# Kernel tuning notes

Hardware: AMD Instinct MI355X
Metric: run time of the kernel (lower is better)

The kernel has to match this reference:

```python
import jax, jax.numpy as jnp
import numpy as np

H, KVH, D = 32, 8, 128          # heads, kv heads, head dim
WINDOW = 512                     # sliding_window
NEG = -1e30


def _rotate_half(x):
    x1, x2 = jnp.split(x, 2, axis=-1)
    return jnp.concatenate([-x2, x1], axis=-1)


def setup_inputs() -> dict:
    key = jax.random.key(0)
    ks = jax.random.split(key, 6)
    B, S = 4, 1024
    T = B * S
    hidden = H * D  # 4096
    # RoPE tables [max_pos, head_dim]
    inv_freq = 1.0 / (10000.0 ** (jnp.arange(0, D, 2, dtype=jnp.float32) / D))
    freqs = jnp.outer(jnp.arange(S, dtype=jnp.float32), inv_freq)
    emb = jnp.concatenate([freqs, freqs], axis=-1)
    cos, sin = jnp.cos(emb), jnp.sin(emb)
    x = jax.random.normal(ks[0], (T, hidden), dtype=jnp.float32)
    pos = jnp.tile(jnp.arange(S, dtype=jnp.int64), B)            # positions restart per seq
    cu = jnp.arange(B + 1, dtype=jnp.int32) * S                  # uniform varlen offsets
    sc = 0.02
    Wq = jax.random.normal(ks[1], (hidden, H * D), jnp.float32) * sc
    Wk = jax.random.normal(ks[2], (hidden, KVH * D), jnp.float32) * sc
    Wv = jax.random.normal(ks[3], (hidden, KVH * D), jnp.float32) * sc
    Wo = jax.random.normal(ks[4], (H * D, hidden), jnp.float32) * sc
    return {"cos": cos, "sin": sin, "nz_hidden_states": x,
            "nz_position_ids": pos, "cu_seqlens": cu, "max_seqlen": S,
            "Wq": Wq, "Wk": Wk, "Wv": Wv, "Wo": Wo}


def reference(cos, sin, nz_hidden_states, nz_position_ids, cu_seqlens, max_seqlen,
              Wq, Wk, Wv, Wo):
    T = nz_hidden_states.shape[0]
    q = (nz_hidden_states @ Wq).reshape(T, H, D)
    k = (nz_hidden_states @ Wk).reshape(T, KVH, D)
    v = (nz_hidden_states @ Wv).reshape(T, KVH, D)
    # RoPE: gather by position, broadcast over head dim (unsqueeze(-2))
    c = cos[nz_position_ids][:, None, :]
    s = sin[nz_position_ids][:, None, :]
    q = q * c + _rotate_half(q) * s
    k = k * c + _rotate_half(k) * s
    # uniform varlen -> batch view [B, S, ...]
    B = cu_seqlens.shape[0] - 1
    S = T // B
    G = H // KVH  # query heads per kv head (GQA)
    qb = q.reshape(B, S, KVH, G, D)
    kb = k.reshape(B, S, KVH, D)
    vb = v.reshape(B, S, KVH, D)
    scores = jnp.einsum('bqhgd,bkhd->bhgqk', qb, kb) / jnp.sqrt(jnp.float32(D))
    i = jnp.arange(S)[:, None]
    j = jnp.arange(S)[None, :]
    mask = (j <= i) & (i - j <= WINDOW)  # causal + sliding window
    scores = jnp.where(mask, scores, NEG)
    p = jax.nn.softmax(scores, axis=-1)
    out = jnp.einsum('bhgqk,bkhd->bqhgd', p, vb).reshape(T, H * D)
    return out @ Wo
```

## Files before the change

kernel.cpp:

```cpp
#include <hip/hip_runtime.h>

typedef __bf16 bf16_t;
typedef __bf16 bf16x8 __attribute__((ext_vector_type(8)));
typedef __bf16 bf16x4 __attribute__((ext_vector_type(4)));
typedef float  f32x4  __attribute__((ext_vector_type(4)));
typedef float  f32x16 __attribute__((ext_vector_type(16)));
typedef unsigned int u32x4 __attribute__((ext_vector_type(4)));

#define N_HEADS 32
#define N_KVH   8
#define HEADDIM 128
#define WINDOW  512
#define NBATCH  4
#define SEQLEN  1024
#define NTOK    (NBATCH * SEQLEN)
#define HIDDEN  4096
#define QKVW    6144

__device__ __forceinline__ void llds16(const bf16_t* g, const bf16_t* l)
{
    __builtin_amdgcn_global_load_lds(
        (const __attribute__((address_space(1))) void*)g,
        (__attribute__((address_space(3))) void*)l, 16, 0, 0);
}

template<bool OUT_F32>
__global__ __launch_bounds__(512, 4)
void gemm_dual_kernel(const bf16_t* __restrict__ A, const bf16_t* __restrict__ Bt,
                      void* __restrict__ Cp, int M, int N, int K)
{
    __shared__ __align__(16) char lds[3 * 24576];
    const int tid  = threadIdx.x;
    const int w    = tid >> 6, lane = tid & 63;
    const int ntx  = N >> 7;
    const int nwg  = gridDim.x;
    const int cpx  = nwg >> 3;
    const int lin  = blockIdx.x;
    const int swz  = (nwg & 7) == 0 ? (lin & 7) * cpx + (lin >> 3) : lin;
    const int m0   = (swz / ntx) * 256;
    const int n0   = (swz % ntx) * 128;
    const int wm   = (w >> 1) * 64;
    const int wn   = (w & 1) * 64;
    const int fr   = lane & 15;
    const int kslot16 = (((lane >> 4) ^ ((lane >> 1) & 3)) << 4);
    const int srcblk  = (((tid & 3) ^ ((tid >> 3) & 3)) << 3);
    const int nk = K >> 5;

    f32x4 acc[4][4];
#pragma unroll
    for (int i = 0; i < 4; ++i)
#pragma unroll
        for (int j = 0; j < 4; ++j) {
            acc[i][j][0] = 0.f; acc[i][j][1] = 0.f;
            acc[i][j][2] = 0.f; acc[i][j][3] = 0.f;
        }

    const bf16_t* arow = A  + (size_t)(m0 + (tid >> 2)) * K + srcblk;
    const bf16_t* brow = Bt + (size_t)(n0 + (tid >> 2)) * K + srcblk;
    const size_t rowK128 = (size_t)128 * K;

    auto STAGE = [&](int tt, int buf) {
        char* dst = lds + buf * 24576 + w * 1024;
        const int kt = tt << 5;
        llds16(arow + kt,           (const bf16_t*)(dst));
        llds16(arow + rowK128 + kt, (const bf16_t*)(dst + 8192));
        llds16(brow + kt,           (const bf16_t*)(dst + 16384));
    };

    STAGE(0, 0); STAGE(1, 1);

    int cur = 0;
    for (int t = 0; t < nk; ++t) {
        if (t + 1 < nk) asm volatile("s_waitcnt vmcnt(3)" ::: "memory");
        else            asm volatile("s_waitcnt vmcnt(0)" ::: "memory");
        __builtin_amdgcn_sched_barrier(0);
        __builtin_amdgcn_s_barrier();
        __builtin_amdgcn_sched_barrier(0);

        const char* base = lds + cur * 24576;
        bf16x8 af[4], bfg[4];
#pragma unroll
        for (int mt = 0; mt < 4; ++mt)
            af[mt] = *(const bf16x8*)(base + ((wm + mt * 16 + fr) << 6) + kslot16);
#pragma unroll
        for (int nt = 0; nt < 4; ++nt)
            bfg[nt] = *(const bf16x8*)(base + 16384 + ((wn + nt * 16 + fr) << 6) + kslot16);

        if (t + 2 < nk) {
            int nb = cur + 2; if (nb >= 3) nb -= 3;
            STAGE(t + 2, nb);
        }
        __builtin_amdgcn_s_setprio(1);
#pragma unroll
        for (int mt = 0; mt < 4; ++mt)
#pragma unroll
            for (int nt = 0; nt < 4; ++nt)
                acc[mt][nt] = __builtin_amdgcn_mfma_f32_16x16x32_bf16(
                    af[mt], bfg[nt], acc[mt][nt], 0, 0, 0);
        __builtin_amdgcn_s_setprio(0);
        ++cur; if (cur == 3) cur = 0;
    }

    const int r0 = (lane >> 4) << 2;
#pragma unroll
    for (int mt = 0; mt < 4; ++mt)
#pragma unroll
        for (int nt = 0; nt < 4; ++nt)
#pragma unroll
            for (int r = 0; r < 4; ++r) {
                int row = m0 + wm + mt * 16 + r0 + r;
                int col = n0 + wn + nt * 16 + fr;
                if constexpr (OUT_F32)
                    ((float*)Cp)[(size_t)row * N + col] = acc[mt][nt][r];
                else
                    ((bf16_t*)Cp)[(size_t)row * N + col] = (bf16_t)acc[mt][nt][r];
            }
}

template<bool A_F32, bool OUT_F32>
__global__ __launch_bounds__(256)
void gemm_kernel(const void* __restrict__ Ap, const void* __restrict__ Bp,
                 void* __restrict__ Cp, int M, int N, int K)
{
    __shared__ bf16_t As[128 * 40];
    __shared__ bf16_t Bs[128 * 40];
    const int tid  = threadIdx.x;
    const int m0   = blockIdx.y * 128;
    const int n0   = blockIdx.x * 128;
    const int wave = tid >> 6, lane = tid & 63;
    const int wm   = (wave >> 1) * 64, wn = (wave & 1) * 64;
    const int fr   = lane & 15;
    const int koff = (lane >> 4) * 8;

    f32x4 acc[4][4];
#pragma unroll
    for (int i = 0; i < 4; ++i)
#pragma unroll
        for (int j = 0; j < 4; ++j) {
            acc[i][j][0] = 0.f; acc[i][j][1] = 0.f;
            acc[i][j][2] = 0.f; acc[i][j][3] = 0.f;
        }

    for (int kt = 0; kt < K; kt += 32) {
        __syncthreads();
        if constexpr (A_F32) {
            const float* A = (const float*)Ap;
#pragma unroll
            for (int i = 0; i < 4; ++i) {
                int lin = tid + i * 256;
                int row = lin >> 3;
                int kq  = (lin & 7) << 2;
                const float4 v = *(const float4*)(A + (size_t)(m0 + row) * K + kt + kq);
                bf16_t* d = &As[row * 40 + kq];
                d[0] = (bf16_t)v.x; d[1] = (bf16_t)v.y;
                d[2] = (bf16_t)v.z; d[3] = (bf16_t)v.w;
            }
        } else {
            const bf16_t* A = (const bf16_t*)Ap;
#pragma unroll
            for (int i = 0; i < 2; ++i) {
                int lin = tid + i * 256;
                int row = lin >> 2;
                int kq  = (lin & 3) << 3;
                *(bf16x8*)&As[row * 40 + kq] =
                    *(const bf16x8*)(A + (size_t)(m0 + row) * K + kt + kq);
            }
        }
        {
            const float* B = (const float*)Bp;
#pragma unroll
            for (int i = 0; i < 4; ++i) {
                int lin = tid + i * 256;
                int kr  = lin >> 5;
                int nc  = (lin & 31) << 2;
                const float4 v = *(const float4*)(B + (size_t)(kt + kr) * N + n0 + nc);
                Bs[(nc + 0) * 40 + kr] = (bf16_t)v.x;
                Bs[(nc + 1) * 40 + kr] = (bf16_t)v.y;
                Bs[(nc + 2) * 40 + kr] = (bf16_t)v.z;
                Bs[(nc + 3) * 40 + kr] = (bf16_t)v.w;
            }
        }
        __syncthreads();
        bf16x8 af[4], bfg[4];
#pragma unroll
        for (int mt = 0; mt < 4; ++mt)
            af[mt] = *(const bf16x8*)&As[(wm + mt * 16 + fr) * 40 + koff];
#pragma unroll
        for (int nt = 0; nt < 4; ++nt)
            bfg[nt] = *(const bf16x8*)&Bs[(wn + nt * 16 + fr) * 40 + koff];
#pragma unroll
        for (int mt = 0; mt < 4; ++mt)
#pragma unroll
            for (int nt = 0; nt < 4; ++nt)
                acc[mt][nt] = __builtin_amdgcn_mfma_f32_16x16x32_bf16(
                    af[mt], bfg[nt], acc[mt][nt], 0, 0, 0);
    }
    const int r0 = (lane >> 4) << 2;
#pragma unroll
    for (int mt = 0; mt < 4; ++mt)
#pragma unroll
        for (int nt = 0; nt < 4; ++nt)
#pragma unroll
            for (int r = 0; r < 4; ++r) {
                int row = m0 + wm + mt * 16 + r0 + r;
                int col = n0 + wn + nt * 16 + fr;
                if constexpr (OUT_F32)
                    ((float*)Cp)[(size_t)row * N + col] = acc[mt][nt][r];
                else
                    ((bf16_t*)Cp)[(size_t)row * N + col] = (bf16_t)acc[mt][nt][r];
            }
}

__global__ __launch_bounds__(256)
void prep_kernel(const float* __restrict__ x,
                 const float* __restrict__ Wq, const float* __restrict__ Wk,
                 const float* __restrict__ Wv, const float* __restrict__ Wo,
                 bf16_t* __restrict__ Xb, bf16_t* __restrict__ Wqkvt,
                 bf16_t* __restrict__ WoT)
{
    __shared__ bf16_t tile[32][33];
    const int bid = blockIdx.x;
    if (bid < 8192) {
        int i = bid * 256 + threadIdx.x;
        const float4 a = *(const float4*)(x + (size_t)i * 8);
        const float4 b = *(const float4*)(x + (size_t)i * 8 + 4);
        bf16x8 v;
        v[0] = (bf16_t)a.x; v[1] = (bf16_t)a.y; v[2] = (bf16_t)a.z; v[3] = (bf16_t)a.w;
        v[4] = (bf16_t)b.x; v[5] = (bf16_t)b.y; v[6] = (bf16_t)b.z; v[7] = (bf16_t)b.w;
        *(bf16x8*)(Xb + (size_t)i * 8) = v;
        return;
    }
    const float* W; bf16_t* Wt; int j;
    if (bid < 24576)      { W = Wq; Wt = Wqkvt;                          j = bid - 8192; }
    else if (bid < 28672) { W = Wk; Wt = Wqkvt + (size_t)4096 * HIDDEN;  j = bid - 24576; }
    else if (bid < 32768) { W = Wv; Wt = Wqkvt + (size_t)5120 * HIDDEN;  j = bid - 28672; }
    else                  { W = Wo; Wt = WoT;                            j = bid - 32768; }
    const int N  = (bid >= 24576 && bid < 32768) ? 1024 : HIDDEN;
    const int k0 = (j & 127) << 5;
    const int n0 = (j >> 7) << 5;
    const int c  = threadIdx.x & 31, r0 = threadIdx.x >> 5;
#pragma unroll
    for (int i = 0; i < 4; ++i) {
        int r = r0 + i * 8;
        tile[r][c] = (bf16_t)W[(size_t)(k0 + r) * N + n0 + c];
    }
    __syncthreads();
#pragma unroll
    for (int i = 0; i < 4; ++i) {
        int r = r0 + i * 8;
        Wt[(size_t)(n0 + r) * HIDDEN + k0 + c] = tile[c][r];
    }
}

__global__ __launch_bounds__(256)
void wtrans_kernel(const float* __restrict__ W, bf16_t* __restrict__ Wt, int K, int N)
{
    __shared__ bf16_t tile[32][33];
    const int k0 = blockIdx.x * 32;
    const int n0 = blockIdx.y * 32;
    const int c  = threadIdx.x & 31, r0 = threadIdx.x >> 5;
#pragma unroll
    for (int i = 0; i < 4; ++i) {
        int r = r0 + i * 8;
        tile[r][c] = (bf16_t)W[(size_t)(k0 + r) * N + n0 + c];
    }
    __syncthreads();
#pragma unroll
    for (int i = 0; i < 4; ++i) {
        int r = r0 + i * 8;
        Wt[(size_t)(n0 + r) * K + k0 + c] = tile[c][r];
    }
}

__global__ __launch_bounds__(256)
void ropek_vtrans_kernel(bf16_t* __restrict__ kb, int kstr,
                         const bf16_t* __restrict__ Vs, int vstr,
                         bf16_t* __restrict__ Vt,
                         const float* __restrict__ cosT, const float* __restrict__ sinT)
{
    __shared__ bf16_t tile[32][33];
    const int bid = blockIdx.x;
    if (bid < 8192) {
        int lin  = bid * 256 + threadIdx.x;
        int d    = lin & 63;
        int rest = lin >> 6;
        int kvh  = rest & 7;
        int t    = rest >> 3;
        int p    = t & (SEQLEN - 1);
        float c = cosT[p * HEADDIM + d];
        float s = sinT[p * HEADDIM + d];
        bf16_t* ptr = kb + (size_t)t * kstr + kvh * HEADDIM;
        float x1 = (float)ptr[d], x2 = (float)ptr[d + 64];
        ptr[d]      = (bf16_t)(x1 * c - x2 * s);
        ptr[d + 64] = (bf16_t)(x2 * c + x1 * s);
        return;
    }
    int j = bid - 8192;
    const int s0  = (j & 31) * 32;
    const int d0  = ((j >> 5) & 3) * 32;
    const int bk  = j >> 7;
    const int b   = bk >> 3, kvh = bk & 7;
    const int c   = threadIdx.x & 31, r0 = threadIdx.x >> 5;
    const bf16_t* src = Vs + (size_t)(b * SEQLEN + s0) * vstr + kvh * HEADDIM + d0;
#pragma unroll
    for (int i = 0; i < 4; ++i) {
        int r = r0 + i * 8;
        tile[r][c] = src[(size_t)r * vstr + c];
    }
    __syncthreads();
    bf16_t* dst = Vt + ((size_t)(b * N_KVH + kvh) * HEADDIM + d0) * SEQLEN + s0;
#pragma unroll
    for (int i = 0; i < 4; ++i) {
        int dr = r0 + i * 8;
        dst[(size_t)dr * SEQLEN + c] = tile[c][dr];
    }
}

__device__ __forceinline__ unsigned int pk2(float a, float b)
{
    unsigned short x = __builtin_bit_cast(unsigned short, (bf16_t)a);
    unsigned short y = __builtin_bit_cast(unsigned short, (bf16_t)b);
    return ((unsigned int)y << 16) | (unsigned int)x;
}
__device__ __forceinline__ void swap32(unsigned int& a, unsigned int& b)
{
    asm volatile("v_permlane32_swap_b32 %0, %1" : "+v"(a), "+v"(b));
}

__device__ __forceinline__ void stage_kv(const bf16_t* __restrict__ Kb, int kstr,
                                         const bf16_t* __restrict__ Vt,
                                         char* ldsb, int bb, int kvh, int kb,
                                         int w, int i)
{
#pragma unroll
    for (int j = 0; j < 2; ++j) {
        int row = w * 8 + j * 4 + (i >> 4);
        const bf16_t* src = Kb + (size_t)(bb * SEQLEN + kb + row) * kstr + kvh * HEADDIM
                          + (((i & 15) ^ (row & 7)) << 3);
        llds16(src, (const bf16_t*)(ldsb + (w * 8 + j * 4) * 256));
    }
#pragma unroll
    for (int j = 0; j < 2; ++j) {
        int d = w * 16 + j * 8 + (i >> 3);
        const bf16_t* src = Vt + ((size_t)((bb * N_KVH + kvh) * HEADDIM + d)) * SEQLEN + kb
                          + (((i & 7) ^ (d & 7)) << 3);
        llds16(src, (const bf16_t*)(ldsb + 16384 + (w * 16 + j * 8) * 128));
    }
}

__global__ __launch_bounds__(512, 2)
void attn32_kernel(const bf16_t* __restrict__ Qb, const bf16_t* __restrict__ Kb,
                   const bf16_t* __restrict__ Vt, bf16_t* __restrict__ Ob,
                   int qstr, int kstr,
                   const float* __restrict__ cosT, const float* __restrict__ sinT)
{
    __shared__ __align__(16) char lds[65536];
    const int tid = threadIdx.x, w = tid >> 6, i = tid & 63;
    const int la = i & 31, hi = i >> 5;
    const int qt = blockIdx.x, kvh = blockIdx.y, bb = blockIdx.z;
    const int Q0 = qt * 64;
    const int h  = kvh * 4 + (w >> 1);
    const int qw = Q0 + 32 * (w & 1);
    const int KL = Q0 >= WINDOW ? Q0 - WINDOW : 0;
    const int nt = (Q0 - KL) / 64 + 1;
    const int iq = qw + la;

    const bf16_t* qp = Qb + (size_t)(bb * SEQLEN + iq) * qstr + h * HEADDIM + 8 * hi;
    bf16x8 qf[8];
#pragma unroll
    for (int c = 0; c < 8; ++c) qf[c] = *(const bf16x8*)(qp + c * 16);

    {
        const float sc = 0.08838834764831845f;
        const float* crow = cosT + (size_t)iq * HEADDIM + 8 * hi;
        const float* srow = sinT + (size_t)iq * HEADDIM + 8 * hi;
#pragma unroll
        for (int c = 0; c < 4; ++c) {
            float4 c0 = *(const float4*)(crow + c * 16);
            float4 c1 = *(const float4*)(crow + c * 16 + 4);
            float4 sA = *(const float4*)(srow + c * 16);
            float4 sB = *(const float4*)(srow + c * 16 + 4);
            float cc[8] = {c0.x, c0.y, c0.z, c0.w, c1.x, c1.y, c1.z, c1.w};
            float ss[8] = {sA.x, sA.y, sA.z, sA.w, sB.x, sB.y, sB.z, sB.w};
#pragma unroll
            for (int j = 0; j < 8; ++j) {
                float x1 = (float)qf[c][j], x2 = (float)qf[c + 4][j];
                qf[c][j]     = (bf16_t)((x1 * cc[j] - x2 * ss[j]) * sc);
                qf[c + 4][j] = (bf16_t)((x2 * cc[j] + x1 * ss[j]) * sc);
            }
        }
    }

    f32x16 oacc[4];
#pragma unroll
    for (int d = 0; d < 4; ++d)
#pragma unroll
        for (int r = 0; r < 16; ++r) oacc[d][r] = 0.f;
    float mrow = -1e30f, lsum = 0.f;

    stage_kv(Kb, kstr, Vt, lds, bb, kvh, KL, w, i);

    const int cswz = (la & 7) << 4;

    for (int t = 0; t < nt; ++t) {
        asm volatile("s_waitcnt vmcnt(0) lgkmcnt(0)" ::: "memory");
        __builtin_amdgcn_sched_barrier(0);
        __syncthreads();
        if (t + 1 < nt)
            stage_kv(Kb, kstr, Vt, lds + ((t + 1) & 1) * 32768, bb, kvh, KL + (t + 1) * 64, w, i);
        const char* KsB = lds + (t & 1) * 32768;
        const char* VsB = KsB + 16384;
        const int kb = KL + t * 64;

        f32x16 s0, s1;
#pragma unroll
        for (int r = 0; r < 16; ++r) { s0[r] = 0.f; s1[r] = 0.f; }
        __builtin_amdgcn_s_setprio(1);
#pragma unroll
        for (int c = 0; c < 8; ++c) {
            bf16x8 k0 = *(const bf16x8*)(KsB + la * 256        + ((c * 32 + 16 * hi) ^ cswz));
            bf16x8 k1 = *(const bf16x8*)(KsB + (la + 32) * 256 + ((c * 32 + 16 * hi) ^ cswz));
            s0 = __builtin_amdgcn_mfma_f32_32x32x16_bf16(k0, qf[c], s0, 0, 0, 0);
            s1 = __builtin_amdgcn_mfma_f32_32x32x16_bf16(k1, qf[c], s1, 0, 0, 0);
        }
        __builtin_amdgcn_s_setprio(0);

        const bool interior = (kb + 63 <= qw) && (kb >= qw - (WINDOW - 31));
        if (!interior) {
#pragma unroll
            for (int r = 0; r < 16; ++r) {
                int j0 = kb + (r & 3) + 8 * (r >> 2) + 4 * hi;
                int j1 = j0 + 32;
                if (!(j0 <= iq && iq - j0 <= WINDOW)) s0[r] = -1e30f;
                if (!(j1 <= iq && iq - j1 <= WINDOW)) s1[r] = -1e30f;
            }
        }

        float mt = fmaxf(s0[0], s1[0]);
#pragma unroll
        for (int r = 1; r < 16; ++r) mt = fmaxf(mt, fmaxf(s0[r], s1[r]));
        mt = fmaxf(mt, __shfl_xor(mt, 32, 64));
        float mnew = fmaxf(mrow, mt);
        float corr = __expf(mrow - mnew);
        float ps = 0.f;
#pragma unroll
        for (int r = 0; r < 16; ++r) {
            s0[r] = __expf(s0[r] - mnew);
            s1[r] = __expf(s1[r] - mnew);
            ps += s0[r] + s1[r];
        }
        ps += __shfl_xor(ps, 32, 64);
        lsum = lsum * corr + ps;
        mrow = mnew;
#pragma unroll
        for (int d = 0; d < 4; ++d)
#pragma unroll
            for (int r = 0; r < 16; ++r) oacc[d][r] *= corr;

        bf16x8 pa[4];
        {
            unsigned int w0 = pk2(s0[0], s0[1]),  w1 = pk2(s0[2], s0[3]);
            unsigned int w2 = pk2(s0[4], s0[5]),  w3 = pk2(s0[6], s0[7]);
            swap32(w0, w2); swap32(w1, w3);
            u32x4 u; u[0] = w0; u[1] = w1; u[2] = w2; u[3] = w3;
            pa[0] = __builtin_bit_cast(bf16x8, u);
            w0 = pk2(s0[8], s0[9]);   w1 = pk2(s0[10], s0[11]);
            w2 = pk2(s0[12], s0[13]); w3 = pk2(s0[14], s0[15]);
            swap32(w0, w2); swap32(w1, w3);
            u[0] = w0; u[1] = w1; u[2] = w2; u[3] = w3;
            pa[1] = __builtin_bit_cast(bf16x8, u);
            w0 = pk2(s1[0], s1[1]);  w1 = pk2(s1[2], s1[3]);
            w2 = pk2(s1[4], s1[5]);  w3 = pk2(s1[6], s1[7]);
            swap32(w0, w2); swap32(w1, w3);
            u[0] = w0; u[1] = w1; u[2] = w2; u[3] = w3;
            pa[2] = __builtin_bit_cast(bf16x8, u);
            w0 = pk2(s1[8], s1[9]);   w1 = pk2(s1[10], s1[11]);
            w2 = pk2(s1[12], s1[13]); w3 = pk2(s1[14], s1[15]);
            swap32(w0, w2); swap32(w1, w3);
            u[0] = w0; u[1] = w1; u[2] = w2; u[3] = w3;
            pa[3] = __builtin_bit_cast(bf16x8, u);
        }

        __builtin_amdgcn_s_setprio(1);
#pragma unroll
        for (int d = 0; d < 4; ++d) {
            const char* vrow = VsB + (d * 32 + la) * 128;
#pragma unroll
            for (int ks = 0; ks < 4; ++ks) {
                bf16x8 vf = *(const bf16x8*)(vrow + ((ks * 32 + 16 * hi) ^ cswz));
                oacc[d] = __builtin_amdgcn_mfma_f32_32x32x16_bf16(vf, pa[ks], oacc[d], 0, 0, 0);
            }
        }
        __builtin_amdgcn_s_setprio(0);
    }

    float rn = 1.f / lsum;
    bf16_t* orow = Ob + ((size_t)((bb * SEQLEN + iq) * N_HEADS + h)) * HEADDIM;
#pragma unroll
    for (int d = 0; d < 4; ++d)
#pragma unroll
        for (int g = 0; g < 4; ++g) {
            bf16x4 v;
            v[0] = (bf16_t)(oacc[d][4 * g + 0] * rn);
            v[1] = (bf16_t)(oacc[d][4 * g + 1] * rn);
            v[2] = (bf16_t)(oacc[d][4 * g + 2] * rn);
            v[3] = (bf16_t)(oacc[d][4 * g + 3] * rn);
            *(bf16x4*)(orow + d * 32 + 8 * g + 4 * hi) = v;
        }
}

extern "C" void kernel_launch(void* const* d_in, const int* in_sizes, int n_in,
                              void* d_out, int out_size, void* d_ws, size_t ws_size,
                              hipStream_t stream)
{
    const float* cosT = (const float*)d_in[0];
    const float* sinT = (const float*)d_in[1];
    const float* x    = (const float*)d_in[2];
    const float* Wq   = (const float*)d_in[6];
    const float* Wk   = (const float*)d_in[7];
    const float* Wv   = (const float*)d_in[8];
    const float* Wo   = (const float*)d_in[9];
    float* out = (float*)d_out;
    char* ws = (char*)d_ws;
    const size_t MB = 1024ull * 1024ull;

    if (ws_size >= 136 * MB) {
        bf16_t* Xb    = (bf16_t*)(ws);
        bf16_t* Wqkvt = (bf16_t*)(ws + 32 * MB);
        bf16_t* QKVb  = (bf16_t*)(ws + 80 * MB);
        bf16_t* Vt    = (bf16_t*)(ws + 128 * MB);
        bf16_t* Ob    = Xb;
        const bool withWo = ws_size >= 168 * MB;
        bf16_t* WoT = withWo ? (bf16_t*)(ws + 136 * MB) : Wqkvt;

        const int prep_blocks = 8192 + 16384 + 4096 + 4096 + (withWo ? 16384 : 0);
        prep_kernel<<<prep_blocks, 256, 0, stream>>>(x, Wq, Wk, Wv, Wo, Xb, Wqkvt, WoT);
        gemm_dual_kernel<false><<<dim3((NTOK/256) * (QKVW/128)), 512, 0, stream>>>(Xb, Wqkvt, QKVb, NTOK, QKVW, HIDDEN);
        if (!withWo)
            wtrans_kernel<<<dim3(HIDDEN/32, HIDDEN/32), 256, 0, stream>>>(Wo, Wqkvt, HIDDEN, HIDDEN);
        ropek_vtrans_kernel<<<8192 + 4096, 256, 0, stream>>>(QKVb + 4096, QKVW, QKVb + 5120, QKVW, Vt, cosT, sinT);
        attn32_kernel<<<dim3(SEQLEN/64, N_KVH, NBATCH), 512, 0, stream>>>(QKVb, QKVb + 4096, Vt, Ob, QKVW, QKVW, cosT, sinT);
        gemm_dual_kernel<true><<<dim3((NTOK/256) * (HIDDEN/128)), 512, 0, stream>>>(Ob, WoT, out, NTOK, HIDDEN, HIDDEN);
    } else {
        bf16_t* Qb = (bf16_t*)(ws);
        bf16_t* Kb = (bf16_t*)(ws + 32 * MB);
        bf16_t* Vb = (bf16_t*)(ws + 40 * MB);
        bf16_t* Vt = (bf16_t*)(ws + 48 * MB);
        bf16_t* Ob = (bf16_t*)(ws + 56 * MB);
        gemm_kernel<true, false><<<dim3(32, 32), 256, 0, stream>>>(x, Wq, Qb, NTOK, HIDDEN, HIDDEN);
        gemm_kernel<true, false><<<dim3(8, 32), 256, 0, stream>>>(x, Wk, Kb, NTOK, 1024, HIDDEN);
        gemm_kernel<true, false><<<dim3(8, 32), 256, 0, stream>>>(x, Wv, Vb, NTOK, 1024, HIDDEN);
        ropek_vtrans_kernel<<<8192 + 4096, 256, 0, stream>>>(Kb, 1024, Vb, 1024, Vt, cosT, sinT);
        attn32_kernel<<<dim3(SEQLEN/64, N_KVH, NBATCH), 512, 0, stream>>>(Qb, Kb, Vt, Ob, HIDDEN, 1024, cosT, sinT);
        gemm_kernel<false, true><<<dim3(32, 32), 256, 0, stream>>>(Ob, Wo, out, NTOK, HIDDEN, HIDDEN);
    }
}
```

Measured before the change: 502.8 us.

## Add 256x256-tile 8-wave GEMM with phased LDS ping-pong for QKV and output projections

Introduces a new GEMM kernel using 256x256 output tiles with 8 waves each owning a 128x64 sub-tile, a 64-wide K step, XOR-swizzled LDS rows, and a double-buffered LDS pipeline. Each K iteration is split into four compute phases interleaved with direct global-to-LDS loads and explicit barriers and waitcnts. The QKV projection and output projection both switch to this kernel. Larger tiles are meant to raise arithmetic intensity and overlap loads with MFMA work, at the cost of 128KB of LDS per block, lower occupancy, and fewer workgroups (384 and 256) to cover the GPU.

```diff
diff --git a/kernel.cpp b/kernel.cpp
--- a/kernel.cpp
+++ b/kernel.cpp
@@ -22,6 +22,182 @@
     __builtin_amdgcn_global_load_lds(
         (const __attribute__((address_space(1))) void*)g,
         (__attribute__((address_space(3))) void*)l, 16, 0, 0);
+}
+
+#define MFMA16(a, b, c) __builtin_amdgcn_mfma_f32_16x16x32_bf16((a), (b), (c), 0, 0, 0)
+
+template<bool OUT_F32>
+__global__ __launch_bounds__(512, 2)
+void gemm8p_kernel(const bf16_t* __restrict__ A, const bf16_t* __restrict__ Bt,
+                   void* __restrict__ Cp, int M, int N, int K)
+{
+    __shared__ __align__(16) char lds[131072];
+    const int tid  = threadIdx.x;
+    const int w    = tid >> 6, lane = tid & 63;
+    const int ntx  = N >> 8;
+    const int nwg  = gridDim.x;
+    const int cpx  = nwg >> 3;
+    const int lin  = blockIdx.x;
+    const int swz  = (nwg & 7) == 0 ? (lin & 7) * cpx + (lin >> 3) : lin;
+    const int m0   = (swz / ntx) * 256;
+    const int n0   = (swz % ntx) * 256;
+    const int wm   = (w >> 2) * 128;
+    const int wn   = (w & 3) * 64;
+    const int fr   = lane & 15, g4 = lane >> 4;
+    const int nk   = K >> 6;
+
+    const int sl0 = (((0 + g4) ^ (fr & 7)) << 4);
+    const int sl1 = (((4 + g4) ^ (fr & 7)) << 4);
+    const int rs  = lane >> 3;
+    const int ssb = (((lane & 7) ^ rs) << 3);
+
+    const bf16_t* aS = A  + (size_t)(m0 + w * 16 + rs) * K + ssb;
+    const bf16_t* bS = Bt + (size_t)(n0 + w * 16 + rs) * K + ssb;
+    const size_t h128 = (size_t)128 * K;
+    const size_t j8   = (size_t)8 * K;
+
+    f32x4 acc[8][4];
+#pragma unroll
+    for (int i = 0; i < 8; ++i)
+#pragma unroll
+        for (int j = 0; j < 4; ++j) {
+            acc[i][j][0] = 0.f; acc[i][j][1] = 0.f;
+            acc[i][j][2] = 0.f; acc[i][j][3] = 0.f;
+        }
+
+    auto STG = [&](int buf, int which, int t) {
+        char* dst = lds + buf * 65536 + which * 16384 + w * 2048;
+        const bf16_t* src = ((which < 2) ? aS : bS)
+                          + (size_t)(which & 1) * h128 + ((size_t)t << 6);
+        llds16(src,      (const bf16_t*)dst);
+        llds16(src + j8, (const bf16_t*)(dst + 1024));
+    };
+
+    STG(0, 0, 0); STG(0, 1, 0); STG(0, 2, 0); STG(0, 3, 0);
+    if (nk > 1) {
+        STG(1, 2, 1); STG(1, 3, 1);
+        asm volatile("s_waitcnt vmcnt(4)" ::: "memory");
+    } else {
+        asm volatile("s_waitcnt vmcnt(0)" ::: "memory");
+    }
+    __builtin_amdgcn_sched_barrier(0);
+    __builtin_amdgcn_s_barrier();
+    __builtin_amdgcn_sched_barrier(0);
+
+    bf16x8 aq[4][2], bl[2][2], bh[2][2];
+
+    for (int t = 0; t < nk; ++t) {
+        const int X = t & 1;
+        const char* Ab = lds + X * 65536;
+        const char* Bb = Ab + 32768;
+
+#pragma unroll
+        for (int mt = 0; mt < 4; ++mt) {
+            const char* p = Ab + (wm + mt * 16 + fr) * 128;
+            aq[mt][0] = *(const bf16x8*)(p + sl0);
+            aq[mt][1] = *(const bf16x8*)(p + sl1);
+        }
+#pragma unroll
+        for (int nt = 0; nt < 2; ++nt) {
+            const char* p = Bb + (wn + nt * 16 + fr) * 128;
+            bl[nt][0] = *(const bf16x8*)(p + sl0);
+            bl[nt][1] = *(const bf16x8*)(p + sl1);
+        }
+        if (t + 1 < nk) STG(1 - X, 0, t + 1);
+        __builtin_amdgcn_s_barrier();
+        asm volatile("s_waitcnt lgkmcnt(0)" ::: "memory");
+        __builtin_amdgcn_sched_barrier(0);
+        __builtin_amdgcn_s_setprio(1);
+#pragma unroll
+        for (int mt = 0; mt < 4; ++mt)
+#pragma unroll
+            for (int nt = 0; nt < 2; ++nt) {
+                acc[mt][nt] = MFMA16(aq[mt][0], bl[nt][0], acc[mt][nt]);
+                acc[mt][nt] = MFMA16(aq[mt][1], bl[nt][1], acc[mt][nt]);
+            }
+        __builtin_amdgcn_s_setprio(0);
+        __builtin_amdgcn_s_barrier();
+        __builtin_amdgcn_sched_barrier(0);
+
+#pragma unroll
+        for (int nt = 0; nt < 2; ++nt) {
+            const char* p = Bb + (wn + (nt + 2) * 16 + fr) * 128;
+            bh[nt][0] = *(const bf16x8*)(p + sl0);
+            bh[nt][1] = *(const bf16x8*)(p + sl1);
+        }
+        if (t + 1 < nk) STG(1 - X, 1, t + 1);
+        __builtin_amdgcn_s_barrier();
+        asm volatile("s_waitcnt lgkmcnt(0)" ::: "memory");
+        __builtin_amdgcn_sched_barrier(0);
+        __builtin_amdgcn_s_setprio(1);
+#pragma unroll
+        for (int mt = 0; mt < 4; ++mt)
+#pragma unroll
+            for (int nt = 0; nt < 2; ++nt) {
+                acc[mt][nt + 2] = MFMA16(aq[mt][0], bh[nt][0], acc[mt][nt + 2]);
+                acc[mt][nt + 2] = MFMA16(aq[mt][1], bh[nt][1], acc[mt][nt + 2]);
+            }
+        __builtin_amdgcn_s_setprio(0);
+        __builtin_amdgcn_s_barrier();
+        __builtin_amdgcn_sched_barrier(0);
+
+#pragma unroll
+        for (int mt = 0; mt < 4; ++mt) {
+            const char* p = Ab + (wm + (mt + 4) * 16 + fr) * 128;
+            aq[mt][0] = *(const bf16x8*)(p + sl0);
+            aq[mt][1] = *(const bf16x8*)(p + sl1);
+        }
+        if (t + 2 < nk) STG(X, 2, t + 2);
+        __builtin_amdgcn_s_barrier();
+        asm volatile("s_waitcnt lgkmcnt(0)" ::: "memory");
+        __builtin_amdgcn_sched_barrier(0);
+        __builtin_amdgcn_s_setprio(1);
+#pragma unroll
+        for (int mt = 0; mt < 4; ++mt)
+#pragma unroll
+            for (int nt = 0; nt < 2; ++nt) {
+                acc[mt + 4][nt] = MFMA16(aq[mt][0], bl[nt][0], acc[mt + 4][nt]);
+                acc[mt + 4][nt] = MFMA16(aq[mt][1], bl[nt][1], acc[mt + 4][nt]);
+            }
+        __builtin_amdgcn_s_setprio(0);
+        __builtin_amdgcn_s_barrier();
+        __builtin_amdgcn_sched_barrier(0);
+
+        if (t + 2 < nk) STG(X, 3, t + 2);
+        __builtin_amdgcn_s_barrier();
+        __builtin_amdgcn_sched_barrier(0);
+        __builtin_amdgcn_s_setprio(1);
+#pragma unroll
+        for (int mt = 0; mt < 4; ++mt)
+#pragma unroll
+            for (int nt = 0; nt < 2; ++nt) {
+                acc[mt + 4][nt + 2] = MFMA16(aq[mt][0], bh[nt][0], acc[mt + 4][nt + 2]);
+                acc[mt + 4][nt + 2] = MFMA16(aq[mt][1], bh[nt][1], acc[mt + 4][nt + 2]);
+            }
+        __builtin_amdgcn_s_setprio(0);
+        if (t + 1 < nk) {
+            if (t + 2 < nk) asm volatile("s_waitcnt vmcnt(4)" ::: "memory");
+            else            asm volatile("s_waitcnt vmcnt(0)" ::: "memory");
+        }
+        __builtin_amdgcn_sched_barrier(0);
+        __builtin_amdgcn_s_barrier();
+        __builtin_amdgcn_sched_barrier(0);
+    }
+
+    const int r0 = g4 << 2;
+#pragma unroll
+    for (int mt = 0; mt < 8; ++mt)
+#pragma unroll
+        for (int nt = 0; nt < 4; ++nt)
+#pragma unroll
+            for (int r = 0; r < 4; ++r) {
+                int row = m0 + wm + mt * 16 + r0 + r;
+                int col = n0 + wn + nt * 16 + fr;
+                if constexpr (OUT_F32)
+                    ((float*)Cp)[(size_t)row * N + col] = acc[mt][nt][r];
+                else
+                    ((bf16_t*)Cp)[(size_t)row * N + col] = (bf16_t)acc[mt][nt][r];
+            }
 }
 
 template<bool OUT_F32>
@@ -95,8 +271,7 @@
         for (int mt = 0; mt < 4; ++mt)
 #pragma unroll
             for (int nt = 0; nt < 4; ++nt)
-                acc[mt][nt] = __builtin_amdgcn_mfma_f32_16x16x32_bf16(
-                    af[mt], bfg[nt], acc[mt][nt], 0, 0, 0);
+                acc[mt][nt] = MFMA16(af[mt], bfg[nt], acc[mt][nt]);
         __builtin_amdgcn_s_setprio(0);
         ++cur; if (cur == 3) cur = 0;
     }
@@ -192,8 +367,7 @@
         for (int mt = 0; mt < 4; ++mt)
 #pragma unroll
             for (int nt = 0; nt < 4; ++nt)
-                acc[mt][nt] = __builtin_amdgcn_mfma_f32_16x16x32_bf16(
-                    af[mt], bfg[nt], acc[mt][nt], 0, 0, 0);
+                acc[mt][nt] = MFMA16(af[mt], bfg[nt], acc[mt][nt]);
     }
     const int r0 = (lane >> 4) << 2;
 #pragma unroll
@@ -535,12 +709,12 @@
 
         const int prep_blocks = 8192 + 16384 + 4096 + 4096 + (withWo ? 16384 : 0);
         prep_kernel<<<prep_blocks, 256, 0, stream>>>(x, Wq, Wk, Wv, Wo, Xb, Wqkvt, WoT);
-        gemm_dual_kernel<false><<<dim3((NTOK/256) * (QKVW/128)), 512, 0, stream>>>(Xb, Wqkvt, QKVb, NTOK, QKVW, HIDDEN);
+        gemm8p_kernel<false><<<dim3((NTOK/256) * (QKVW/256)), 512, 0, stream>>>(Xb, Wqkvt, QKVb, NTOK, QKVW, HIDDEN);
         if (!withWo)
             wtrans_kernel<<<dim3(HIDDEN/32, HIDDEN/32), 256, 0, stream>>>(Wo, Wqkvt, HIDDEN, HIDDEN);
         ropek_vtrans_kernel<<<8192 + 4096, 256, 0, stream>>>(QKVb + 4096, QKVW, QKVb + 5120, QKVW, Vt, cosT, sinT);
         attn32_kernel<<<dim3(SEQLEN/64, N_KVH, NBATCH), 512, 0, stream>>>(QKVb, QKVb + 4096, Vt, Ob, QKVW, QKVW, cosT, sinT);
-        gemm_dual_kernel<true><<<dim3((NTOK/256) * (HIDDEN/128)), 512, 0, stream>>>(Ob, WoT, out, NTOK, HIDDEN, HIDDEN);
+        gemm8p_kernel<true><<<dim3((NTOK/256) * (HIDDEN/256)), 512, 0, stream>>>(Ob, WoT, out, NTOK, HIDDEN, HIDDEN);
     } else {
         bf16_t* Qb = (bf16_t*)(ws);
         bf16_t* Kb = (bf16_t*)(ws + 32 * MB);
```

Result: faster. 492.8 us (-2.0%).
